# Optimization experiments

Hardware: AMD Instinct MI355X
Metric: run time of the kernel (lower is better)

## Reference

```python
import jax, jax.numpy as jnp
import numpy as np

NEG_SLOPE = 0.2


def gat_conv(x, src, dst, W, a_src, a_dst, bias, n_nodes):
    # PyG GATConv (heads=1): h = xW; e_ij = LeakyReLU(a_src.h_j + a_dst.h_i)
    # softmax over incoming edges per destination node, then scatter-sum.
    h = x @ W                                  # [N, F]
    alpha_s = h @ a_src                        # [N]
    alpha_d = h @ a_dst                        # [N]
    e = jax.nn.leaky_relu(alpha_s[src] + alpha_d[dst], NEG_SLOPE)  # [E]
    m = jax.ops.segment_max(e, dst, num_segments=n_nodes)
    ex = jnp.exp(e - m[dst])
    denom = jax.ops.segment_sum(ex, dst, num_segments=n_nodes)
    alpha = ex / denom[dst]                    # [E]
    out = jax.ops.segment_sum(alpha[:, None] * h[src], dst, num_segments=n_nodes)
    return out + bias


def setup_inputs() -> dict:
    key = jax.random.key(0)
    ks = jax.random.split(key, 16)
    N, E, F_in = 50000, 800000, 256
    x = jax.random.normal(ks[0], (N, F_in), dtype=jnp.float32)
    edge_index = jax.random.randint(ks[1], (2, E), 0, N, dtype=jnp.int64)

    def glorot(k, shape):
        fan_in, fan_out = shape[0], shape[-1]
        s = jnp.sqrt(6.0 / (fan_in + fan_out))
        return jax.random.uniform(k, shape, jnp.float32, -s, s)

    params = dict(
        W1=glorot(ks[2], (F_in, 128)),
        a1s=glorot(ks[3], (128,)),
        a1d=glorot(ks[4], (128,)),
        b1=jnp.zeros((128,), jnp.float32),
        Wl=glorot(ks[5], (128, 32)),
        bl=jnp.zeros((32,), jnp.float32),
        W2=glorot(ks[6], (32, 16)),
        a2s=glorot(ks[7], (16,)),
        a2d=glorot(ks[8], (16,)),
        b2=jnp.zeros((16,), jnp.float32),
        Wm=glorot(ks[9], (16, 1)),
        bm=jnp.zeros((1,), jnp.float32),
    )
    return {"x": x, "edge_index": edge_index, **params}


def reference(x, edge_index, W1, a1s, a1d, b1, Wl, bl, W2, a2s, a2d, b2, Wm, bm):
    n = x.shape[0]
    loops = jnp.arange(n, dtype=edge_index.dtype)
    src = jnp.concatenate([edge_index[0], loops])  # add_self_loops=True
    dst = jnp.concatenate([edge_index[1], loops])

    h = jax.nn.relu(gat_conv(x, src, dst, W1, a1s, a1d, b1, n))
    h = h @ Wl + bl
    h = jax.nn.relu(gat_conv(h, src, dst, W2, a2s, a2d, b2, n))
    out = h @ Wm + bm                             # MLP([16,1]) = single Linear
    return out.squeeze()
```

## Files before the change

### kernel.cpp

```cpp
#include <hip/hip_runtime.h>
#include <math.h>


#define NEG_SLOPE 0.2f

#define BSHIFT 8
#define BCAP   6144
#define BCAPC  (BCAP + 256)

typedef __attribute__((ext_vector_type(8))) short bf16x8;
typedef __attribute__((ext_vector_type(4))) float f32x4;
typedef __attribute__((ext_vector_type(8))) _Float16 h16x8;

__device__ __forceinline__ unsigned short bf_hi(float f) {
    unsigned u = __float_as_uint(f);
    return (unsigned short)((u + 0x7fffu + ((u >> 16) & 1u)) >> 16);
}
__device__ __forceinline__ float bf_tof(unsigned short s) {
    return __uint_as_float(((unsigned)s) << 16);
}


__launch_bounds__(256)
__global__ void k_bin(const int* __restrict__ src_e, const int* __restrict__ dst_e,
                      int E, int* __restrict__ gcur, unsigned* __restrict__ binned) {
    __shared__ int scnt[256];
    __shared__ int sbase[256];
    int tid = threadIdx.x;
    scnt[tid] = 0;
    __syncthreads();
    int base_e = blockIdx.x * 4096;
    int myd[16];
#pragma unroll
    for (int k = 0; k < 16; ++k) {
        int j = base_e + k * 256 + tid;
        if (j < E) {
            int d = dst_e[j];
            myd[k] = d;
            atomicAdd(&scnt[d >> BSHIFT], 1);
        } else myd[k] = -1;
    }
    __syncthreads();
    int c = scnt[tid];
    sbase[tid] = c ? atomicAdd(&gcur[tid], c) : 0;
    scnt[tid] = 0;
    __syncthreads();
#pragma unroll
    for (int k = 0; k < 16; ++k) {
        int j = base_e + k * 256 + tid;
        if (j >= E) continue;
        int d = myd[k];
        int b = d >> BSHIFT;
        int off = sbase[b] + atomicAdd(&scnt[b], 1);
        if (off < BCAP)
            binned[(size_t)b * BCAP + off] = ((unsigned)src_e[j] << BSHIFT) | (unsigned)(d & 255);
    }
}

__launch_bounds__(256)
__global__ void k_csr(const unsigned* __restrict__ binned, const int* __restrict__ gcur,
                      int N, int* __restrict__ csr, int* __restrict__ rowptr,
                      int* __restrict__ rowend) {
    __shared__ int sdeg[256], s[256], scur[256];
    int b = blockIdx.x, tid = threadIdx.x;
    int node0 = b << BSHIFT;
    int nloc = N - node0; if (nloc > 256) nloc = 256;
    int cnt = gcur[b]; if (cnt > BCAP) cnt = BCAP;
    sdeg[tid] = (tid < nloc) ? 1 : 0;
    __syncthreads();
    const unsigned* bp = binned + (size_t)b * BCAP;
    for (int j = tid; j < cnt; j += 256) atomicAdd(&sdeg[bp[j] & 255], 1);
    __syncthreads();
    int v = sdeg[tid];
    s[tid] = v;
    __syncthreads();
    for (int off = 1; off < 256; off <<= 1) {
        int t = (tid >= off) ? s[tid - off] : 0;
        __syncthreads();
        s[tid] += t;
        __syncthreads();
    }
    int excl = s[tid] - v;
    int rowbase = b * BCAPC;
    if (tid < nloc) {
        rowptr[node0 + tid] = rowbase + excl;
        rowend[node0 + tid] = rowbase + excl + v;
        csr[rowbase + excl] = node0 + tid;
    }
    scur[tid] = excl + 1;
    __syncthreads();
    for (int j = tid; j < cnt; j += 256) {
        unsigned p = bp[j];
        int pos = atomicAdd(&scur[p & 255], 1);
        csr[rowbase + pos] = (int)(p >> BSHIFT);
    }
}


__global__ void k_wcvt(const float* __restrict__ W, short* __restrict__ Wt_hi,
                       short* __restrict__ Wt_lo) {
    int i = blockIdx.x * 256 + threadIdx.x;
    int k = i >> 7, c = i & 127;
    float v = W[i];
    unsigned short h = bf_hi(v);
    unsigned short l = bf_hi(v - bf_tof(h));
    Wt_hi[c * 256 + k] = (short)h;
    Wt_lo[c * 256 + k] = (short)l;
}


#define LDST 40

__launch_bounds__(256)
__global__ void k_gemm1_mfma(const float* __restrict__ x, const short* __restrict__ Wt_hi,
                             const short* __restrict__ Wt_lo,
                             const float* __restrict__ a1s, const float* __restrict__ a1d,
                             int N, _Float16* __restrict__ h1h,
                             float* __restrict__ as1, float* __restrict__ ad1) {
    __shared__ short Ah[64 * LDST], Al[64 * LDST];
    __shared__ short Bh[128 * LDST], Bl[128 * LDST];
    int tid = threadIdx.x;
    int w = tid >> 6, lane = tid & 63;
    int rowbase = blockIdx.x * 64;

    f32x4 acc[8];
#pragma unroll
    for (int c = 0; c < 8; ++c) acc[c] = (f32x4){0.f, 0.f, 0.f, 0.f};

    int arow = tid >> 2;
    int aq   = tid & 3;
    int agrow = rowbase + arow;
    int fr = lane & 15;
    int fk = lane >> 4;

    for (int ks = 0; ks < 8; ++ks) {
        int k0 = ks * 32;
        __syncthreads();
        {
            float4 u0 = make_float4(0.f, 0.f, 0.f, 0.f), u1 = u0;
            if (agrow < N) {
                const float* p = x + (size_t)agrow * 256 + k0 + aq * 8;
                u0 = *(const float4*)p;
                u1 = *(const float4*)(p + 4);
            }
            float f[8] = {u0.x, u0.y, u0.z, u0.w, u1.x, u1.y, u1.z, u1.w};
            bf16x8 hv, lv;
#pragma unroll
            for (int j = 0; j < 8; ++j) {
                unsigned short h = bf_hi(f[j]);
                unsigned short l = bf_hi(f[j] - bf_tof(h));
                hv[j] = (short)h;
                lv[j] = (short)l;
            }
            *(bf16x8*)&Ah[arow * LDST + aq * 8] = hv;
            *(bf16x8*)&Al[arow * LDST + aq * 8] = lv;
        }
        {
#pragma unroll
            for (int rep = 0; rep < 2; ++rep) {
                int ci = tid + rep * 256;
                int row = ci >> 2, q = ci & 3;
                const short* ph = Wt_hi + row * 256 + k0 + q * 8;
                const short* pl = Wt_lo + row * 256 + k0 + q * 8;
                *(bf16x8*)&Bh[row * LDST + q * 8] = *(const bf16x8*)ph;
                *(bf16x8*)&Bl[row * LDST + q * 8] = *(const bf16x8*)pl;
            }
        }
        __syncthreads();
        bf16x8 a_h = *(const bf16x8*)&Ah[(w * 16 + fr) * LDST + fk * 8];
        bf16x8 a_l = *(const bf16x8*)&Al[(w * 16 + fr) * LDST + fk * 8];
#pragma unroll
        for (int c = 0; c < 8; ++c) {
            bf16x8 b_h = *(const bf16x8*)&Bh[(c * 16 + fr) * LDST + fk * 8];
            bf16x8 b_l = *(const bf16x8*)&Bl[(c * 16 + fr) * LDST + fk * 8];
            acc[c] = __builtin_amdgcn_mfma_f32_16x16x32_bf16(a_h, b_h, acc[c], 0, 0, 0);
            acc[c] = __builtin_amdgcn_mfma_f32_16x16x32_bf16(a_l, b_h, acc[c], 0, 0, 0);
            acc[c] = __builtin_amdgcn_mfma_f32_16x16x32_bf16(a_h, b_l, acc[c], 0, 0, 0);
        }
    }

    float s_[4] = {0.f, 0.f, 0.f, 0.f};
    float d_[4] = {0.f, 0.f, 0.f, 0.f};
#pragma unroll
    for (int c = 0; c < 8; ++c) {
        int col = c * 16 + fr;
        float av = a1s[col], dv = a1d[col];
#pragma unroll
        for (int r = 0; r < 4; ++r) {
            s_[r] += acc[c][r] * av;
            d_[r] += acc[c][r] * dv;
        }
    }
#pragma unroll
    for (int off = 1; off < 16; off <<= 1) {
#pragma unroll
        for (int r = 0; r < 4; ++r) {
            s_[r] += __shfl_xor(s_[r], off);
            d_[r] += __shfl_xor(d_[r], off);
        }
    }
#pragma unroll
    for (int r = 0; r < 4; ++r) {
        int grow = rowbase + w * 16 + fk * 4 + r;
        if (grow < N) {
            _Float16* dst = h1h + (size_t)grow * 128;
#pragma unroll
            for (int c = 0; c < 8; ++c) dst[c * 16 + fr] = (_Float16)acc[c][r];
        }
    }
    if (fr == 0) {
#pragma unroll
        for (int r = 0; r < 4; ++r) {
            int grow = rowbase + w * 16 + fk * 4 + r;
            if (grow < N) { as1[grow] = s_[r]; ad1[grow] = d_[r]; }
        }
    }
}


__global__ void k_agg1(const _Float16* __restrict__ h1h, const float* __restrict__ as1,
                       const float* __restrict__ ad1, const int* __restrict__ rowptr,
                       const int* __restrict__ rowend,
                       const int* __restrict__ csr_src, const float* __restrict__ b1,
                       int N, float* __restrict__ out1) {
    int wid = (blockIdx.x * blockDim.x + threadIdx.x) >> 6;
    int lane = threadIdx.x & 63;
    if (wid >= N) return;
    int beg = rowptr[wid], end = rowend[wid];
    float adn = ad1[wid];

    int g = lane >> 4;
    int f8 = lane & 15;
    float acc[8];
#pragma unroll
    for (int k = 0; k < 8; ++k) acc[k] = 0.f;
    float den = 0.f;

    int j = beg + g;
    for (; j + 4 < end; j += 8) {
        int s0 = csr_src[j];
        int s1 = csr_src[j + 4];
        h16x8 v0 = *(const h16x8*)(h1h + (size_t)s0 * 128 + f8 * 8);
        h16x8 v1 = *(const h16x8*)(h1h + (size_t)s1 * 128 + f8 * 8);
        float e0 = as1[s0] + adn; e0 = e0 > 0.f ? e0 : NEG_SLOPE * e0;
        float e1 = as1[s1] + adn; e1 = e1 > 0.f ? e1 : NEG_SLOPE * e1;
        float w0 = __expf(e0), w1 = __expf(e1);
        den += w0 + w1;
#pragma unroll
        for (int k = 0; k < 8; ++k)
            acc[k] += w0 * (float)v0[k] + w1 * (float)v1[k];
    }
    if (j < end) {
        int s0 = csr_src[j];
        h16x8 v0 = *(const h16x8*)(h1h + (size_t)s0 * 128 + f8 * 8);
        float e0 = as1[s0] + adn; e0 = e0 > 0.f ? e0 : NEG_SLOPE * e0;
        float w0 = __expf(e0);
        den += w0;
#pragma unroll
        for (int k = 0; k < 8; ++k) acc[k] += w0 * (float)v0[k];
    }
#pragma unroll
    for (int off = 16; off <= 32; off <<= 1) {
#pragma unroll
        for (int k = 0; k < 8; ++k) acc[k] += __shfl_xor(acc[k], off);
        den += __shfl_xor(den, off);
    }
    if (g == 0) {
        float inv = 1.f / den;
        float o[8];
        const float* bb = b1 + f8 * 8;
#pragma unroll
        for (int k = 0; k < 8; ++k) o[k] = fmaxf(acc[k] * inv + bb[k], 0.f);
        float* dst = out1 + (size_t)wid * 128 + f8 * 8;
        *(float4*)dst = make_float4(o[0], o[1], o[2], o[3]);
        *(float4*)(dst + 4) = make_float4(o[4], o[5], o[6], o[7]);
    }
}


__launch_bounds__(256)
__global__ void k_mlp(const float* __restrict__ out1, const float* __restrict__ Wl,
                      const float* __restrict__ bl, const float* __restrict__ W2,
                      const float* __restrict__ a2s, const float* __restrict__ a2d,
                      int N, float* __restrict__ h3,
                      float* __restrict__ as2, float* __restrict__ ad2) {
    __shared__ float sWl[128 * 32];
    __shared__ float sW2[32 * 16];
    __shared__ float sbl[32];
    __shared__ float sa2s[16];
    __shared__ float sa2d[16];
    int tid = threadIdx.x;
    for (int i = tid; i < 128 * 32; i += blockDim.x) sWl[i] = Wl[i];
    for (int i = tid; i < 32 * 16; i += blockDim.x) sW2[i] = W2[i];
    if (tid < 32) sbl[tid] = bl[tid];
    if (tid < 16) { sa2s[tid] = a2s[tid]; sa2d[tid] = a2d[tid]; }
    __syncthreads();
    int n = blockIdx.x * blockDim.x + tid;
    if (n >= N) return;

    float h2[32];
#pragma unroll
    for (int j = 0; j < 32; ++j) h2[j] = sbl[j];
    const float4* row = (const float4*)(out1 + (size_t)n * 128);
    for (int k4 = 0; k4 < 32; ++k4) {
        float4 v = row[k4];
        const float* w0 = &sWl[(k4 * 4 + 0) * 32];
        const float* w1 = &sWl[(k4 * 4 + 1) * 32];
        const float* w2 = &sWl[(k4 * 4 + 2) * 32];
        const float* w3 = &sWl[(k4 * 4 + 3) * 32];
#pragma unroll
        for (int j = 0; j < 32; ++j)
            h2[j] += v.x * w0[j] + v.y * w1[j] + v.z * w2[j] + v.w * w3[j];
    }
    float h3l[16];
#pragma unroll
    for (int j = 0; j < 16; ++j) h3l[j] = 0.f;
#pragma unroll
    for (int k = 0; k < 32; ++k) {
        float hv = h2[k];
#pragma unroll
        for (int j = 0; j < 16; ++j) h3l[j] += hv * sW2[k * 16 + j];
    }
    float s = 0.f, d = 0.f;
#pragma unroll
    for (int j = 0; j < 16; ++j) { s += h3l[j] * sa2s[j]; d += h3l[j] * sa2d[j]; }
    float4* h3row = (float4*)(h3 + (size_t)n * 16);
    h3row[0] = make_float4(h3l[0], h3l[1], h3l[2], h3l[3]);
    h3row[1] = make_float4(h3l[4], h3l[5], h3l[6], h3l[7]);
    h3row[2] = make_float4(h3l[8], h3l[9], h3l[10], h3l[11]);
    h3row[3] = make_float4(h3l[12], h3l[13], h3l[14], h3l[15]);
    as2[n] = s;
    ad2[n] = d;
}


__global__ void k_agg2(const float* __restrict__ h3, const float* __restrict__ as2,
                       const float* __restrict__ ad2, const int* __restrict__ rowptr,
                       const int* __restrict__ rowend,
                       const int* __restrict__ csr_src, const float* __restrict__ b2,
                       const float* __restrict__ Wm, const float* __restrict__ bm,
                       int N, float* __restrict__ out) {
    int wid = (blockIdx.x * blockDim.x + threadIdx.x) >> 6;
    int lane = threadIdx.x & 63;
    if (wid >= N) return;
    int beg = rowptr[wid], end = rowend[wid];
    float adn = ad2[wid];

    int eg = lane >> 2;
    int f4 = lane & 3;
    float4 acc = make_float4(0.f, 0.f, 0.f, 0.f);
    float den = 0.f;
    for (int j = beg + eg; j < end; j += 16) {
        int s = csr_src[j];
        float e = as2[s] + adn;
        e = e > 0.f ? e : NEG_SLOPE * e;
        float w = __expf(e);
        den += w;
        float4 v = ((const float4*)(h3 + (size_t)s * 16))[f4];
        acc.x += w * v.x; acc.y += w * v.y;
        acc.z += w * v.z; acc.w += w * v.w;
    }
#pragma unroll
    for (int off = 4; off <= 32; off <<= 1) {
        acc.x += __shfl_xor(acc.x, off);
        acc.y += __shfl_xor(acc.y, off);
        acc.z += __shfl_xor(acc.z, off);
        acc.w += __shfl_xor(acc.w, off);
        den   += __shfl_xor(den, off);
    }
    float inv = 1.f / den;
    float4 bb = ((const float4*)b2)[f4];
    float4 wm = ((const float4*)Wm)[f4];
    float o0 = fmaxf(acc.x * inv + bb.x, 0.f);
    float o1 = fmaxf(acc.y * inv + bb.y, 0.f);
    float o2 = fmaxf(acc.z * inv + bb.z, 0.f);
    float o3 = fmaxf(acc.w * inv + bb.w, 0.f);
    float v = o0 * wm.x + o1 * wm.y + o2 * wm.z + o3 * wm.w;
    v += __shfl_xor(v, 1);
    v += __shfl_xor(v, 2);
    if (lane == 0) out[wid] = v + bm[0];
}


extern "C" void kernel_launch(void* const* d_in, const int* in_sizes, int n_in,
                              void* d_out, int out_size, void* d_ws, size_t ws_size,
                              hipStream_t stream) {
    const float* x   = (const float*)d_in[0];
    const int*   ei  = (const int*)d_in[1];
    const float* W1  = (const float*)d_in[2];
    const float* a1s = (const float*)d_in[3];
    const float* a1d = (const float*)d_in[4];
    const float* b1  = (const float*)d_in[5];
    const float* Wl  = (const float*)d_in[6];
    const float* bl  = (const float*)d_in[7];
    const float* W2  = (const float*)d_in[8];
    const float* a2s = (const float*)d_in[9];
    const float* a2d = (const float*)d_in[10];
    const float* b2  = (const float*)d_in[11];
    const float* Wm  = (const float*)d_in[12];
    const float* bm  = (const float*)d_in[13];

    int N  = in_sizes[0] / 256;
    int E  = in_sizes[1] / 2;
    int nbuck = (N + 255) >> BSHIFT;
    float* out = (float*)d_out;

    char* w = (char*)d_ws;
    auto alloc = [&](size_t bytes) -> char* {
        char* p = w;
        w += (bytes + 255) & ~(size_t)255;
        return p;
    };
    _Float16* h1h = (_Float16*)alloc((size_t)N * 128 * 2);
    float* out1   = (float*)alloc((size_t)N * 128 * 4);
    float* h3     = (float*)alloc((size_t)N * 16 * 4);
    float* as1    = (float*)alloc((size_t)N * 4);
    float* ad1    = (float*)alloc((size_t)N * 4);
    float* as2    = (float*)alloc((size_t)N * 4);
    float* ad2    = (float*)alloc((size_t)N * 4);
    int*   rowptr = (int*)alloc((size_t)N * 4);
    int*   rowend = (int*)alloc((size_t)N * 4);
    int*   gcur   = (int*)alloc(256 * 4);
    short* Wt_hi  = (short*)alloc((size_t)128 * 256 * 2);
    short* Wt_lo  = (short*)alloc((size_t)128 * 256 * 2);
    unsigned* binned = (unsigned*)alloc((size_t)nbuck * BCAP * 4);
    int*   csr    = (int*)alloc((size_t)nbuck * BCAPC * 4);

    const int* src_e = ei;
    const int* dst_e = ei + E;

    hipMemsetAsync(gcur, 0, 256 * 4, stream);
    k_bin<<<(E + 4095) / 4096, 256, 0, stream>>>(src_e, dst_e, E, gcur, binned);
    k_csr<<<nbuck, 256, 0, stream>>>(binned, gcur, N, csr, rowptr, rowend);

    k_wcvt<<<128, 256, 0, stream>>>(W1, Wt_hi, Wt_lo);
    k_gemm1_mfma<<<(N + 63) / 64, 256, 0, stream>>>(x, Wt_hi, Wt_lo, a1s, a1d,
                                                    N, h1h, as1, ad1);
    k_agg1<<<(N + 3) / 4, 256, 0, stream>>>(h1h, as1, ad1, rowptr, rowend, csr, b1, N, out1);
    k_mlp<<<(N + 255) / 256, 256, 0, stream>>>(out1, Wl, bl, W2, a2s, a2d, N, h3, as2, ad2);
    k_agg2<<<(N + 3) / 4, 256, 0, stream>>>(h3, as2, ad2, rowptr, rowend, csr, b2, Wm, bm, N, out);
}
```

Baseline: 147.1 us.

## Precompute normalized attention weights per edge in separate kernel before aggregation

Adds a k_wexp kernel that computes per-edge exp(LeakyReLU) weights and normalizes them by the per-node sum, storing them in a new edge-sized buffer. Both aggregation kernels then read precomputed weights instead of gathering alpha_src and computing exp and the denominator. k_agg1 is also unrolled to four gathered neighbors per group, and the memset becomes a tiny zero kernel. The cost is two extra launches and extra edge-array traffic, and k_wexp runs one thread per node with serial, poorly coalesced loops.

```diff
diff --git a/kernel.cpp b/kernel.cpp
--- a/kernel.cpp
+++ b/kernel.cpp
@@ -19,6 +19,9 @@
 __device__ __forceinline__ float bf_tof(unsigned short s) {
     return __uint_as_float(((unsigned)s) << 16);
 }
+
+
+__global__ void k_zero(int* __restrict__ p) { p[threadIdx.x] = 0; }
 
 
 __launch_bounds__(256)
@@ -94,6 +97,26 @@
         int pos = atomicAdd(&scur[p & 255], 1);
         csr[rowbase + pos] = (int)(p >> BSHIFT);
     }
+}
+
+
+__global__ void k_wexp(const float* __restrict__ asv, const float* __restrict__ adv,
+                       const int* __restrict__ rowptr, const int* __restrict__ rowend,
+                       const int* __restrict__ csr, int N, float* __restrict__ wn) {
+    int n = blockIdx.x * 256 + threadIdx.x;
+    if (n >= N) return;
+    int beg = rowptr[n], end = rowend[n];
+    float adn = adv[n];
+    float den = 0.f;
+    for (int j = beg; j < end; ++j) {
+        float e = asv[csr[j]] + adn;
+        e = e > 0.f ? e : NEG_SLOPE * e;
+        float w = __expf(e);
+        wn[j] = w;
+        den += w;
+    }
+    float inv = 1.f / den;
+    for (int j = beg; j < end; ++j) wn[j] *= inv;
 }
 
 
@@ -218,44 +241,41 @@
 }
 
 
-__global__ void k_agg1(const _Float16* __restrict__ h1h, const float* __restrict__ as1,
-                       const float* __restrict__ ad1, const int* __restrict__ rowptr,
-                       const int* __restrict__ rowend,
-                       const int* __restrict__ csr_src, const float* __restrict__ b1,
+__global__ void k_agg1(const _Float16* __restrict__ h1h, const float* __restrict__ wn,
+                       const int* __restrict__ rowptr, const int* __restrict__ rowend,
+                       const int* __restrict__ csr, const float* __restrict__ b1,
                        int N, float* __restrict__ out1) {
     int wid = (blockIdx.x * blockDim.x + threadIdx.x) >> 6;
     int lane = threadIdx.x & 63;
     if (wid >= N) return;
     int beg = rowptr[wid], end = rowend[wid];
-    float adn = ad1[wid];
 
     int g = lane >> 4;
     int f8 = lane & 15;
     float acc[8];
 #pragma unroll
     for (int k = 0; k < 8; ++k) acc[k] = 0.f;
-    float den = 0.f;
 
     int j = beg + g;
-    for (; j + 4 < end; j += 8) {
-        int s0 = csr_src[j];
-        int s1 = csr_src[j + 4];
+    for (; j + 12 < end; j += 16) {
+        int s0 = csr[j];
+        int s1 = csr[j + 4];
+        int s2 = csr[j + 8];
+        int s3 = csr[j + 12];
+        float w0 = wn[j], w1 = wn[j + 4], w2 = wn[j + 8], w3 = wn[j + 12];
         h16x8 v0 = *(const h16x8*)(h1h + (size_t)s0 * 128 + f8 * 8);
         h16x8 v1 = *(const h16x8*)(h1h + (size_t)s1 * 128 + f8 * 8);
-        float e0 = as1[s0] + adn; e0 = e0 > 0.f ? e0 : NEG_SLOPE * e0;
-        float e1 = as1[s1] + adn; e1 = e1 > 0.f ? e1 : NEG_SLOPE * e1;
-        float w0 = __expf(e0), w1 = __expf(e1);
-        den += w0 + w1;
+        h16x8 v2 = *(const h16x8*)(h1h + (size_t)s2 * 128 + f8 * 8);
+        h16x8 v3 = *(const h16x8*)(h1h + (size_t)s3 * 128 + f8 * 8);
 #pragma unroll
         for (int k = 0; k < 8; ++k)
-            acc[k] += w0 * (float)v0[k] + w1 * (float)v1[k];
-    }
-    if (j < end) {
-        int s0 = csr_src[j];
+            acc[k] += w0 * (float)v0[k] + w1 * (float)v1[k]
+                    + w2 * (float)v2[k] + w3 * (float)v3[k];
+    }
+    for (; j < end; j += 4) {
+        int s0 = csr[j];
+        float w0 = wn[j];
         h16x8 v0 = *(const h16x8*)(h1h + (size_t)s0 * 128 + f8 * 8);
-        float e0 = as1[s0] + adn; e0 = e0 > 0.f ? e0 : NEG_SLOPE * e0;
-        float w0 = __expf(e0);
-        den += w0;
 #pragma unroll
         for (int k = 0; k < 8; ++k) acc[k] += w0 * (float)v0[k];
     }
@@ -263,14 +283,12 @@
     for (int off = 16; off <= 32; off <<= 1) {
 #pragma unroll
         for (int k = 0; k < 8; ++k) acc[k] += __shfl_xor(acc[k], off);
-        den += __shfl_xor(den, off);
     }
     if (g == 0) {
-        float inv = 1.f / den;
+        const float* bb = b1 + f8 * 8;
         float o[8];
-        const float* bb = b1 + f8 * 8;
-#pragma unroll
-        for (int k = 0; k < 8; ++k) o[k] = fmaxf(acc[k] * inv + bb[k], 0.f);
+#pragma unroll
+        for (int k = 0; k < 8; ++k) o[k] = fmaxf(acc[k] + bb[k], 0.f);
         float* dst = out1 + (size_t)wid * 128 + f8 * 8;
         *(float4*)dst = make_float4(o[0], o[1], o[2], o[3]);
         *(float4*)(dst + 4) = make_float4(o[4], o[5], o[6], o[7]);
@@ -334,28 +352,22 @@
 }
 
 
-__global__ void k_agg2(const float* __restrict__ h3, const float* __restrict__ as2,
-                       const float* __restrict__ ad2, const int* __restrict__ rowptr,
-                       const int* __restrict__ rowend,
-                       const int* __restrict__ csr_src, const float* __restrict__ b2,
+__global__ void k_agg2(const float* __restrict__ h3, const float* __restrict__ wn,
+                       const int* __restrict__ rowptr, const int* __restrict__ rowend,
+                       const int* __restrict__ csr, const float* __restrict__ b2,
                        const float* __restrict__ Wm, const float* __restrict__ bm,
                        int N, float* __restrict__ out) {
     int wid = (blockIdx.x * blockDim.x + threadIdx.x) >> 6;
     int lane = threadIdx.x & 63;
     if (wid >= N) return;
     int beg = rowptr[wid], end = rowend[wid];
-    float adn = ad2[wid];
 
     int eg = lane >> 2;
     int f4 = lane & 3;
     float4 acc = make_float4(0.f, 0.f, 0.f, 0.f);
-    float den = 0.f;
     for (int j = beg + eg; j < end; j += 16) {
-        int s = csr_src[j];
-        float e = as2[s] + adn;
-        e = e > 0.f ? e : NEG_SLOPE * e;
-        float w = __expf(e);
-        den += w;
+        int s = csr[j];
+        float w = wn[j];
         float4 v = ((const float4*)(h3 + (size_t)s * 16))[f4];
         acc.x += w * v.x; acc.y += w * v.y;
         acc.z += w * v.z; acc.w += w * v.w;
@@ -366,15 +378,13 @@
         acc.y += __shfl_xor(acc.y, off);
         acc.z += __shfl_xor(acc.z, off);
         acc.w += __shfl_xor(acc.w, off);
-        den   += __shfl_xor(den, off);
-    }
-    float inv = 1.f / den;
+    }
     float4 bb = ((const float4*)b2)[f4];
     float4 wm = ((const float4*)Wm)[f4];
-    float o0 = fmaxf(acc.x * inv + bb.x, 0.f);
-    float o1 = fmaxf(acc.y * inv + bb.y, 0.f);
-    float o2 = fmaxf(acc.z * inv + bb.z, 0.f);
-    float o3 = fmaxf(acc.w * inv + bb.w, 0.f);
+    float o0 = fmaxf(acc.x + bb.x, 0.f);
+    float o1 = fmaxf(acc.y + bb.y, 0.f);
+    float o2 = fmaxf(acc.z + bb.z, 0.f);
+    float o3 = fmaxf(acc.w + bb.w, 0.f);
     float v = o0 * wm.x + o1 * wm.y + o2 * wm.z + o3 * wm.w;
     v += __shfl_xor(v, 1);
     v += __shfl_xor(v, 2);
@@ -425,18 +435,22 @@
     short* Wt_lo  = (short*)alloc((size_t)128 * 256 * 2);
     unsigned* binned = (unsigned*)alloc((size_t)nbuck * BCAP * 4);
     int*   csr    = (int*)alloc((size_t)nbuck * BCAPC * 4);
+    float* wn     = (float*)alloc((size_t)nbuck * BCAPC * 4);
 
     const int* src_e = ei;
     const int* dst_e = ei + E;
 
-    hipMemsetAsync(gcur, 0, 256 * 4, stream);
+    k_zero<<<1, 256, 0, stream>>>(gcur);
     k_bin<<<(E + 4095) / 4096, 256, 0, stream>>>(src_e, dst_e, E, gcur, binned);
     k_csr<<<nbuck, 256, 0, stream>>>(binned, gcur, N, csr, rowptr, rowend);
 
     k_wcvt<<<128, 256, 0, stream>>>(W1, Wt_hi, Wt_lo);
     k_gemm1_mfma<<<(N + 63) / 64, 256, 0, stream>>>(x, Wt_hi, Wt_lo, a1s, a1d,
                                                     N, h1h, as1, ad1);
-    k_agg1<<<(N + 3) / 4, 256, 0, stream>>>(h1h, as1, ad1, rowptr, rowend, csr, b1, N, out1);
-    k_mlp<<<(N + 255) / 256, 256, 0, stream>>>(out1, Wl, bl, W2, a2s, a2d, N, h3, as2, ad2);
-    k_agg2<<<(N + 3) / 4, 256, 0, stream>>>(h3, as2, ad2, rowptr, rowend, csr, b2, Wm, bm, N, out);
-}
+    int NB = (N + 255) / 256;
+    k_wexp<<<NB, 256, 0, stream>>>(as1, ad1, rowptr, rowend, csr, N, wn);
+    k_agg1<<<(N + 3) / 4, 256, 0, stream>>>(h1h, wn, rowptr, rowend, csr, b1, N, out1);
+    k_mlp<<<NB, 256, 0, stream>>>(out1, Wl, bl, W2, a2s, a2d, N, h3, as2, ad2);
+    k_wexp<<<NB, 256, 0, stream>>>(as2, ad2, rowptr, rowend, csr, N, wn);
+    k_agg2<<<(N + 3) / 4, 256, 0, stream>>>(h3, wn, rowptr, rowend, csr, b2, Wm, bm, N, out);
+}
```

Result: slower. 180.4 us (+22.6%).
